# Optimization experiments

Hardware: AMD Instinct MI355X
Metric: run time of the kernel (lower is better)

Reference implementation:

```python
import jax, jax.numpy as jnp
import numpy as np

B, L = 8, 512
D_MODEL, N_HEADS, N_LAYERS = 768, 12, 12
D_HEAD = D_MODEL // N_HEADS
D_FF = 4 * D_MODEL
NUM_LABELS = 1000
PATCH_DIM = 16 * 16 * 3
EPS = 1e-6


def setup_inputs() -> dict:
    key = jax.random.key(0)
    ks = jax.random.split(key, 24)
    d = D_MODEL

    def w(k, shape, fan_in):
        return (jax.random.normal(k, shape, jnp.float32) / np.sqrt(fan_in)).astype(jnp.float32)

    return {
        'patch': jax.random.normal(ks[0], (B, L, PATCH_DIM), jnp.float32),
        'box': jax.random.uniform(ks[1], (B, L, 4), jnp.float32),
        'patch_W': w(ks[2], (PATCH_DIM, d), PATCH_DIM),
        'patch_b': jnp.zeros((d,), jnp.float32),
        'box_W': w(ks[3], (d, d), d),
        'box_b': jnp.zeros((d,), jnp.float32),
        'Wq': w(ks[4], (N_LAYERS, d, d), d),
        'Wk': w(ks[5], (N_LAYERS, d, d), d),
        'Wv': w(ks[6], (N_LAYERS, d, d), d),
        'Wo': w(ks[7], (N_LAYERS, d, d), d),
        'attn_norm_w': jnp.ones((N_LAYERS, d), jnp.float32),
        'gate_W': w(ks[8], (N_LAYERS, d, D_FF), d),
        'hidden_W': w(ks[9], (N_LAYERS, d, D_FF), d),
        'ffn_out_W': w(ks[10], (N_LAYERS, D_FF, d), D_FF),
        'ffn_norm_w': jnp.ones((N_LAYERS, d), jnp.float32),
        'reward_norm_w': jnp.ones((d,), jnp.float32),
        'reward_W': w(ks[11], (d, 2), d),
        'reward_b': jnp.zeros((2,), jnp.float32),
        'label_norm_w': jnp.ones((d,), jnp.float32),
        'label_W': w(ks[12], (d, NUM_LABELS), d),
        'label_b': jnp.zeros((NUM_LABELS,), jnp.float32),
        'box_norm_w': jnp.ones((d,), jnp.float32),
        'boxh_W': w(ks[13], (d, 4), d),
        'boxh_b': jnp.zeros((4,), jnp.float32),
    }


def _rmsnorm(x, wgt):
    return x * jax.lax.rsqrt(jnp.mean(x * x, axis=-1, keepdims=True) + EPS) * wgt


def _rope(x, cos, sin):
    # x: [b, n, l, dh]; consecutive pairs form complex numbers (view_as_complex)
    xr, xi = x[..., 0::2], x[..., 1::2]
    out_r = xr * cos - xi * sin
    out_i = xr * sin + xi * cos
    return jnp.stack((out_r, out_i), axis=-1).reshape(x.shape)


def _forward(patch, box, patch_W, patch_b, box_W, box_b, Wq, Wk, Wv, Wo,
             attn_norm_w, gate_W, hidden_W, ffn_out_W, ffn_norm_w,
             reward_norm_w, reward_W, reward_b, label_norm_w, label_W, label_b,
             box_norm_w, boxh_W, boxh_b):
    b, l, _ = patch.shape
    d = D_MODEL
    # StackedSinusoidalEmbedding(d_model, 4): d_stack = d/4, theta over d_stack/2 freqs
    d_stack = d // 4
    theta_box = 1.0 / (10000.0 ** (2.0 * jnp.arange(d_stack // 2, dtype=jnp.float32) / d_stack))
    ang = box[..., None] * theta_box  # [b, l, 4, d_stack/2]
    box_sin = jnp.stack((jnp.cos(ang), jnp.sin(ang)), axis=-1).reshape(b, l, d)

    x = (patch @ patch_W + patch_b) + (box_sin @ box_W + box_b)

    # RoPE tables and causal mask (constants)
    theta = 1.0 / (10000.0 ** (2.0 * jnp.arange(D_HEAD // 2, dtype=jnp.float32) / D_HEAD))
    pos_ang = jnp.arange(l, dtype=jnp.float32)[:, None] * theta  # [l, dh/2]
    cos, sin = jnp.cos(pos_ang), jnp.sin(pos_ang)
    mask = jnp.triu(jnp.full((l, l), -jnp.inf, dtype=jnp.float32), 1)
    scale = jnp.float32(np.sqrt(D_HEAD))

    def block(h, p):
        wq, wk, wv, wo, anw, gw, hw, ow, fnw = p
        hn = _rmsnorm(h, anw)
        q = (hn @ wq).reshape(b, l, N_HEADS, D_HEAD).transpose(0, 2, 1, 3)
        k = (hn @ wk).reshape(b, l, N_HEADS, D_HEAD).transpose(0, 2, 1, 3)
        v = (hn @ wv).reshape(b, l, N_HEADS, D_HEAD).transpose(0, 2, 1, 3)
        scores = jnp.einsum('bnld,bnmd->bnlm', _rope(q, cos, sin), _rope(k, cos, sin)) / scale
        attn = jax.nn.softmax(scores + mask, axis=-1)
        o = jnp.einsum('bnlm,bnmd->bnld', attn, v).transpose(0, 2, 1, 3).reshape(b, l, d)
        h = h + o @ wo
        hn = _rmsnorm(h, fnw)
        h = h + (jax.nn.silu(hn @ gw) * (hn @ hw)) @ ow
        return h, None

    x, _ = jax.lax.scan(block, x, (Wq, Wk, Wv, Wo, attn_norm_w, gate_W, hidden_W, ffn_out_W, ffn_norm_w))

    reward = _rmsnorm(x, reward_norm_w) @ reward_W + reward_b
    label = _rmsnorm(x, label_norm_w) @ label_W + label_b
    box_out = _rmsnorm(x, box_norm_w) @ boxh_W + boxh_b
    return reward, label, box_out


def reference(patch, box, patch_W, patch_b, box_W, box_b, Wq, Wk, Wv, Wo,
              attn_norm_w, gate_W, hidden_W, ffn_out_W, ffn_norm_w,
              reward_norm_w, reward_W, reward_b, label_norm_w, label_W, label_b,
              box_norm_w, boxh_W, boxh_b):
    return _forward(patch, box, patch_W, patch_b, box_W, box_b, Wq, Wk, Wv, Wo,
                    attn_norm_w, gate_W, hidden_W, ffn_out_W, ffn_norm_w,
                    reward_norm_w, reward_W, reward_b, label_norm_w, label_W, label_b,
                    box_norm_w, boxh_W, boxh_b)
```

## Files before the change

### kernel.cpp

```cpp
#include <hip/hip_runtime.h>
#include <math.h>
#include <type_traits>

#define B_   8
#define L_   512
#define MTOK 4096
#define D_   768
#define NH_  12
#define DH_  64
#define DFF_ 3072
#define NL_  12

typedef unsigned short u16;
typedef __attribute__((ext_vector_type(4))) float f32x4;
typedef __attribute__((ext_vector_type(8))) short i16x8;
typedef __attribute__((ext_vector_type(8))) __bf16 b16x8;

template <typename A, typename = void>
struct PickFrag { using type = i16x8; };
template <typename A>
struct PickFrag<A, std::void_t<decltype(__builtin_amdgcn_mfma_f32_16x16x32_bf16(
    std::declval<A>(), std::declval<A>(), std::declval<f32x4>(), 0, 0, 0))>> {
  using type = A;
};
using frag_t = typename PickFrag<b16x8>::type;

#if __has_builtin(__builtin_amdgcn_global_load_lds)
#define HAS_GLDS 1
#else
#define HAS_GLDS 0
#endif

__device__ inline u16 f2bf(float f) {
    unsigned u = __float_as_uint(f);
    unsigned r = u + 0x7fffu + ((u >> 16) & 1u);
    return (u16)(r >> 16);
}
__device__ inline float bf2f(u16 b) { return __uint_as_float(((unsigned)b) << 16); }

__device__ inline void bar_raw() {
    asm volatile("" ::: "memory");
    __builtin_amdgcn_s_barrier();
    asm volatile("" ::: "memory");
}

__global__ void k_box_sin(u16* __restrict__ emb, const float* __restrict__ box) {
    int idx = blockIdx.x * blockDim.x + threadIdx.x;
    if (idx >= MTOK * D_) return;
    int t = idx / D_, d = idx % D_;
    int c = d / 192, r = d % 192, j = r >> 1;
    float theta = __expf(-(float)j * (9.210340371976184f / 96.0f));
    float ang = box[t * 4 + c] * theta;
    emb[(size_t)t * 1536 + 768 + d] = f2bf((r & 1) ? sinf(ang) : cosf(ang));
}

__global__ void k_cast(u16* __restrict__ emb, const float* __restrict__ in, int n4) {
    int i = blockIdx.x * blockDim.x + threadIdx.x;
    if (i >= n4) return;
    int t = i / 192, c4 = (i % 192) * 4;
    float4 v = *reinterpret_cast<const float4*>(in + (size_t)t * 768 + c4);
    unsigned lo = (unsigned)f2bf(v.x) | ((unsigned)f2bf(v.y) << 16);
    unsigned hi = (unsigned)f2bf(v.z) | ((unsigned)f2bf(v.w) << 16);
    *reinterpret_cast<uint2*>(emb + (size_t)t * 1536 + c4) = make_uint2(lo, hi);
}

__global__ void k_addb(float* __restrict__ dst, const float* __restrict__ a,
                       const float* __restrict__ b) {
    int i = blockIdx.x * blockDim.x + threadIdx.x;
    if (i < D_) dst[i] = a[i] + b[i];
}

__global__ __launch_bounds__(256) void k_convT(u16* __restrict__ dst,
                                               const float* __restrict__ src,
                                               int K, int N, int ld, int rs,
                                               int ro, int co) {
    __shared__ float t[32][33];
    int bn = blockIdx.x * 32;
    int bk = blockIdx.y * 32;
    int tx = threadIdx.x % 32, ty = threadIdx.x / 32;
    #pragma unroll
    for (int i = 0; i < 4; ++i) {
        int k = bk + ty + i * 8;
        int n = bn + tx;
        t[ty + i * 8][tx] = (n < N) ? src[(size_t)k * N + n] : 0.0f;
    }
    __syncthreads();
    #pragma unroll
    for (int i = 0; i < 4; ++i) {
        int n = bn + ty + i * 8;
        int k = bk + tx;
        dst[(size_t)(n * rs + ro) * ld + co + k] = f2bf(t[tx][ty + i * 8]);
    }
}

__global__ __launch_bounds__(256) void k_convT_b1(u16* __restrict__ dst,
                                                  const float* __restrict__ src,
                                                  int K, int N) {
    __shared__ float t[32][33];
    const float* s = src + (size_t)blockIdx.z * K * N;
    u16* d = dst + (size_t)blockIdx.z * K * N;
    int bn = blockIdx.x * 32, bk = blockIdx.y * 32;
    int tx = threadIdx.x % 32, ty = threadIdx.x / 32;
    #pragma unroll
    for (int i = 0; i < 4; ++i)
        t[ty + i * 8][tx] = s[(size_t)(bk + ty + i * 8) * N + bn + tx];
    __syncthreads();
    #pragma unroll
    for (int i = 0; i < 4; ++i) {
        int n = bn + ty + i * 8, k = bk + tx;
        d[(size_t)n * K + k] = f2bf(t[tx][ty + i * 8]);
    }
}

__global__ __launch_bounds__(256) void k_convT_qkv(u16* __restrict__ dst,
                                                   const float* __restrict__ s0,
                                                   const float* __restrict__ s1,
                                                   const float* __restrict__ s2) {
    __shared__ float t[32][33];
    int ly = blockIdx.z / 3, which = blockIdx.z % 3;
    const float* src = (which == 0 ? s0 : (which == 1 ? s1 : s2)) + (size_t)ly * 768 * 768;
    u16* d = dst + ((size_t)ly * 3 + which) * 768 * 768;
    int bn = blockIdx.x * 32, bk = blockIdx.y * 32;
    int tx = threadIdx.x % 32, ty = threadIdx.x / 32;
    #pragma unroll
    for (int i = 0; i < 4; ++i)
        t[ty + i * 8][tx] = src[(size_t)(bk + ty + i * 8) * 768 + bn + tx];
    __syncthreads();
    #pragma unroll
    for (int i = 0; i < 4; ++i) {
        int n = bn + ty + i * 8, k = bk + tx;
        d[(size_t)n * 768 + k] = f2bf(t[tx][ty + i * 8]);
    }
}

__global__ __launch_bounds__(256) void k_convT_gh(u16* __restrict__ dst,
                                                  const float* __restrict__ g,
                                                  const float* __restrict__ h) {
    __shared__ float t[32][33];
    int ly = blockIdx.z >> 1, which = blockIdx.z & 1;
    const float* src = (which ? h : g) + (size_t)ly * 768 * 3072;
    u16* d = dst + (size_t)ly * 6144 * 768;
    int ro = which * 16;
    int bn = blockIdx.x * 32, bk = blockIdx.y * 32;
    int tx = threadIdx.x % 32, ty = threadIdx.x / 32;
    #pragma unroll
    for (int i = 0; i < 4; ++i)
        t[ty + i * 8][tx] = src[(size_t)(bk + ty + i * 8) * 3072 + bn + tx];
    __syncthreads();
    #pragma unroll
    for (int i = 0; i < 4; ++i) {
        int n = bn + ty + i * 8, k = bk + tx;
        int row = ((n >> 4) << 5) + (n & 15) + ro;
        d[(size_t)row * 768 + k] = f2bf(t[tx][ty + i * 8]);
    }
}

__global__ __launch_bounds__(256) void k_rmsnorm(u16* __restrict__ out,
                                                 const float* __restrict__ in,
                                                 const float* __restrict__ w) {
    int t = blockIdx.x;
    const float* x = in + (size_t)t * D_;
    float ss = 0.f;
    for (int i = threadIdx.x; i < D_; i += 256) { float v = x[i]; ss += v * v; }
    for (int off = 32; off > 0; off >>= 1) ss += __shfl_down(ss, off);
    __shared__ float red[4];
    int wid = threadIdx.x >> 6, lane = threadIdx.x & 63;
    if (lane == 0) red[wid] = ss;
    __syncthreads();
    float tot = red[0] + red[1] + red[2] + red[3];
    float inv = rsqrtf(tot / (float)D_ + 1e-6f);
    for (int i = threadIdx.x; i < D_; i += 256)
        out[(size_t)t * D_ + i] = f2bf(x[i] * inv * w[i]);
}

template <int S>
__global__ __launch_bounds__(256) void k_fused_rr(float* __restrict__ h,
                                                  const float* __restrict__ part,
                                                  u16* __restrict__ hn,
                                                  const float* __restrict__ w) {
    int t = blockIdx.x;
    size_t base = (size_t)t * D_;
    float x[3];
    float ss = 0.f;
    #pragma unroll
    for (int c = 0; c < 3; ++c) {
        int i = threadIdx.x + c * 256;
        float v = h[base + i];
        #pragma unroll
        for (int s = 0; s < S; ++s)
            v += part[(size_t)s * MTOK * D_ + base + i];
        x[c] = v;
        h[base + i] = v;
        ss += v * v;
    }
    for (int off = 32; off > 0; off >>= 1) ss += __shfl_down(ss, off);
    __shared__ float red[4];
    int wid = threadIdx.x >> 6, lane = threadIdx.x & 63;
    if (lane == 0) red[wid] = ss;
    __syncthreads();
    float tot = red[0] + red[1] + red[2] + red[3];
    float inv = rsqrtf(tot / (float)D_ + 1e-6f);
    #pragma unroll
    for (int c = 0; c < 3; ++c) {
        int i = threadIdx.x + c * 256;
        hn[base + i] = f2bf(x[c] * inv * w[i]);
    }
}

__global__ void k_rope_tab(float* __restrict__ tab) {
    int idx = blockIdx.x * blockDim.x + threadIdx.x;
    if (idx >= L_ * 32) return;
    int l = idx >> 5, j = idx & 31;
    float theta = __expf(-(float)j * (9.210340371976184f / 32.0f));
    float s, c;
    sincosf((float)l * theta, &s, &c);
    tab[idx * 2] = c;
    tab[idx * 2 + 1] = s;
}

__global__ __launch_bounds__(256) void k_qkvprep(u16* __restrict__ qh,
                                                 u16* __restrict__ kh,
                                                 u16* __restrict__ vT,
                                                 const u16* __restrict__ qkv,
                                                 const float* __restrict__ tab) {
    int bh = blockIdx.x, lb = blockIdx.y;
    int b = bh / NH_, hh = bh % NH_;
    int tid = threadIdx.x;
    int r = tid >> 3, c8 = (tid & 7) * 8;
    int l = lb * 32 + r;
    size_t rowbase = ((size_t)(b * L_ + l)) * 2304 + hh * 64 + c8;

    float2 cs[4];
    #pragma unroll
    for (int p = 0; p < 4; ++p)
        cs[p] = *reinterpret_cast<const float2*>(tab + ((size_t)l * 32 + (c8 >> 1) + p) * 2);

    {
        uint4 v4 = *reinterpret_cast<const uint4*>(qkv + rowbase);
        const u16* pv = reinterpret_cast<const u16*>(&v4);
        u16 out[8];
        #pragma unroll
        for (int p = 0; p < 4; ++p) {
            float xr = bf2f(pv[2 * p]), xi = bf2f(pv[2 * p + 1]);
            out[2 * p]     = f2bf((xr * cs[p].x - xi * cs[p].y) * 0.125f);
            out[2 * p + 1] = f2bf((xr * cs[p].y + xi * cs[p].x) * 0.125f);
        }
        *reinterpret_cast<uint4*>(qh + ((size_t)bh * L_ + l) * 64 + c8) =
            *reinterpret_cast<uint4*>(out);
    }
    {
        uint4 v4 = *reinterpret_cast<const uint4*>(qkv + rowbase + 768);
        const u16* pv = reinterpret_cast<const u16*>(&v4);
        u16 out[8];
        #pragma unroll
        for (int p = 0; p < 4; ++p) {
            float xr = bf2f(pv[2 * p]), xi = bf2f(pv[2 * p + 1]);
            out[2 * p]     = f2bf(xr * cs[p].x - xi * cs[p].y);
            out[2 * p + 1] = f2bf(xr * cs[p].y + xi * cs[p].x);
        }
        *reinterpret_cast<uint4*>(kh + ((size_t)bh * L_ + l) * 64 + c8) =
            *reinterpret_cast<uint4*>(out);
    }
    __shared__ u16 ts[64][40];
    {
        uint4 v4 = *reinterpret_cast<const uint4*>(qkv + rowbase + 1536);
        const u16* pv = reinterpret_cast<const u16*>(&v4);
        #pragma unroll
        for (int j = 0; j < 8; ++j) ts[c8 + j][r] = pv[j];
    }
    __syncthreads();
    {
        int d = tid >> 2, l0 = (tid & 3) * 8;
        uint4 o4 = *reinterpret_cast<const uint4*>(&ts[d][l0]);
        *reinterpret_cast<uint4*>(vT + ((size_t)bh * 64 + d) * L_ + lb * 32 + l0) = o4;
    }
}

template <int MODE>
__global__ __launch_bounds__(256) void k_gemm_bf16(void* __restrict__ Cp,
                                                   const u16* __restrict__ A,
                                                   const u16* __restrict__ BT,
                                                   const float* __restrict__ bias,
                                                   int K, int Nout, int ldC) {
    __shared__ u16 As[2][128 * 32];
    __shared__ u16 Bs[2][128 * 32];
    int tid = threadIdx.x;
    int wid = tid >> 6, lane = tid & 63;

    int nx = gridDim.x, ny = gridDim.y, nz = gridDim.z;
    int bid = ((blockIdx.z * ny) + blockIdx.y) * nx + blockIdx.x;
    int nwg = nx * ny * nz;
    int cpx = nwg >> 3;
    int swz = (bid & 7) * cpx + (bid >> 3);
    int sk  = swz / (nx * ny);
    int rem = swz % (nx * ny);
    int by = rem / nx, bx = rem % nx;
    int row0 = by * 128, col0 = bx * 128;
    int wr = wid >> 1, wc = wid & 1;

    int Klen = K / nz;
    int kbeg = sk * Klen;

    int c0 = wid * 128 + lane;
    int c1 = c0 + 64;
    int r0 = c0 >> 2, kc0 = (c0 & 3) * 8;
    int r1 = c1 >> 2, kc1 = (c1 & 3) * 8;
    const u16* gA0 = A  + (size_t)(row0 + r0) * K + kbeg + kc0;
    const u16* gA1 = A  + (size_t)(row0 + r1) * K + kbeg + kc1;
    const u16* gB0 = BT + (size_t)(col0 + r0) * K + kbeg + kc0;
    const u16* gB1 = BT + (size_t)(col0 + r1) * K + kbeg + kc1;

    auto stage = [&](int buf, int kt) {
#if HAS_GLDS
        __builtin_amdgcn_global_load_lds(
            (const __attribute__((address_space(1))) void*)(gA0 + kt),
            (__attribute__((address_space(3))) void*)&As[buf][c0 * 8], 16, 0, 0);
        __builtin_amdgcn_global_load_lds(
            (const __attribute__((address_space(1))) void*)(gA1 + kt),
            (__attribute__((address_space(3))) void*)&As[buf][c1 * 8], 16, 0, 0);
        __builtin_amdgcn_global_load_lds(
            (const __attribute__((address_space(1))) void*)(gB0 + kt),
            (__attribute__((address_space(3))) void*)&Bs[buf][c0 * 8], 16, 0, 0);
        __builtin_amdgcn_global_load_lds(
            (const __attribute__((address_space(1))) void*)(gB1 + kt),
            (__attribute__((address_space(3))) void*)&Bs[buf][c1 * 8], 16, 0, 0);
#else
        *reinterpret_cast<uint4*>(&As[buf][c0 * 8]) = *reinterpret_cast<const uint4*>(gA0 + kt);
        *reinterpret_cast<uint4*>(&As[buf][c1 * 8]) = *reinterpret_cast<const uint4*>(gA1 + kt);
        *reinterpret_cast<uint4*>(&Bs[buf][c0 * 8]) = *reinterpret_cast<const uint4*>(gB0 + kt);
        *reinterpret_cast<uint4*>(&Bs[buf][c1 * 8]) = *reinterpret_cast<const uint4*>(gB1 + kt);
#endif
    };

    f32x4 acc[4][4] = {};
    int lrow = lane & 15, lk = (lane >> 4) * 8;

    stage(0, 0);
    int cur = 0;
    for (int kt = 0; kt < Klen; kt += 32) {
        bool has_next = (kt + 32 < Klen);
        if (has_next) stage(cur ^ 1, kt + 32);
        if (has_next) asm volatile("s_waitcnt vmcnt(4) lgkmcnt(0)" ::: "memory");
        else          asm volatile("s_waitcnt vmcnt(0) lgkmcnt(0)" ::: "memory");
        __builtin_amdgcn_sched_barrier(0);
        bar_raw();
        frag_t af[4], bfr[4];
        #pragma unroll
        for (int m = 0; m < 4; ++m)
            af[m] = *reinterpret_cast<const frag_t*>(&As[cur][(wr * 64 + m * 16 + lrow) * 32 + lk]);
        #pragma unroll
        for (int n = 0; n < 4; ++n)
            bfr[n] = *reinterpret_cast<const frag_t*>(&Bs[cur][(wc * 64 + n * 16 + lrow) * 32 + lk]);
        #pragma unroll
        for (int m = 0; m < 4; ++m)
            #pragma unroll
            for (int n = 0; n < 4; ++n)
                acc[m][n] = __builtin_amdgcn_mfma_f32_16x16x32_bf16(af[m], bfr[n], acc[m][n], 0, 0, 0);
        bar_raw();
        cur ^= 1;
    }

    int lcol = lane & 15, rb = (lane >> 4) * 4;
    if (MODE == 5) {
        #pragma unroll
        for (int m = 0; m < 4; ++m) {
            #pragma unroll
            for (int np = 0; np < 2; ++np) {
                int ocol = (col0 >> 1) + wc * 32 + np * 16 + lcol;
                #pragma unroll
                for (int e = 0; e < 4; ++e) {
                    int row = row0 + wr * 64 + m * 16 + rb + e;
                    float g = acc[m][2 * np][e], hv = acc[m][2 * np + 1][e];
                    float s = g / (1.0f + __expf(-g));
                    ((u16*)Cp)[(size_t)row * ldC + ocol] = f2bf(s * hv);
                }
            }
        }
        return;
    }

    float* Cpart = (MODE == 4)
        ? ((float*)Cp + (size_t)sk * (size_t)(ny * 128) * ldC) : (float*)Cp;
    #pragma unroll
    for (int m = 0; m < 4; ++m) {
        #pragma unroll
        for (int n = 0; n < 4; ++n) {
            int col = col0 + wc * 64 + n * 16 + lcol;
            if (col >= Nout) continue;
            #pragma unroll
            for (int e = 0; e < 4; ++e) {
                int row = row0 + wr * 64 + m * 16 + rb + e;
                float v = acc[m][n][e];
                size_t off = (size_t)row * ldC + col;
                if (MODE == 0) {
                    if (bias) v += bias[col];
                    ((float*)Cp)[off] = v;
                } else if (MODE == 3) {
                    ((u16*)Cp)[off] = f2bf(v);
                } else if (MODE == 4) {
                    Cpart[off] = v;
                }
            }
        }
    }
}

__global__ __launch_bounds__(256) void k_attn3(u16* __restrict__ o,
                                               const u16* __restrict__ qh,
                                               const u16* __restrict__ kh,
                                               const u16* __restrict__ vT) {
    int bh = blockIdx.x, qb = blockIdx.y;
    int b = bh / NH_, hh = bh % NH_;
    int tid = threadIdx.x, wid = tid >> 6, lane = tid & 63;
    __shared__ u16 Qs[64][72], Ks[64][72], Vs[64][72], Ps[64][72];

    #pragma unroll
    for (int i = 0; i < 2; ++i) {
        int idx = tid + i * 256;
        int r = idx >> 3, c8 = (idx & 7) * 8;
        uint4 v4 = *reinterpret_cast<const uint4*>(
            qh + ((size_t)bh * L_ + qb * 64 + r) * 64 + c8);
        *reinterpret_cast<uint4*>(&Qs[r][c8]) = v4;
    }
    __syncthreads();

    int lr = lane & 15, lg = lane >> 4;
    frag_t aq[2];
    #pragma unroll
    for (int kd = 0; kd < 2; ++kd)
        aq[kd] = *reinterpret_cast<const frag_t*>(&Qs[wid * 16 + lr][kd * 32 + lg * 8]);

    f32x4 accO[4] = {};
    float M[4], S[4];
    #pragma unroll
    for (int e = 0; e < 4; ++e) { M[e] = -INFINITY; S[e] = 0.f; }

    for (int kb = 0; kb <= qb; ++kb) {
        __syncthreads();
        #pragma unroll
        for (int i = 0; i < 2; ++i) {
            int idx = tid + i * 256;
            int r = idx >> 3, c8 = (idx & 7) * 8;
            *reinterpret_cast<uint4*>(&Ks[r][c8]) = *reinterpret_cast<const uint4*>(
                kh + ((size_t)bh * L_ + kb * 64 + r) * 64 + c8);
            *reinterpret_cast<uint4*>(&Vs[r][c8]) = *reinterpret_cast<const uint4*>(
                vT + ((size_t)bh * 64 + r) * L_ + kb * 64 + c8);
        }
        __syncthreads();

        f32x4 sv[4];
        #pragma unroll
        for (int ct = 0; ct < 4; ++ct) {
            frag_t bk0 = *reinterpret_cast<const frag_t*>(&Ks[ct * 16 + lr][lg * 8]);
            frag_t bk1 = *reinterpret_cast<const frag_t*>(&Ks[ct * 16 + lr][32 + lg * 8]);
            f32x4 z = {0.f, 0.f, 0.f, 0.f};
            z = __builtin_amdgcn_mfma_f32_16x16x32_bf16(aq[0], bk0, z, 0, 0, 0);
            sv[ct] = __builtin_amdgcn_mfma_f32_16x16x32_bf16(aq[1], bk1, z, 0, 0, 0);
        }

        bool diag = (kb == qb);
        float esc[4];
        #pragma unroll
        for (int e = 0; e < 4; ++e) {
            int qg = qb * 64 + wid * 16 + lg * 4 + e;
            float mx = -1e30f;
            #pragma unroll
            for (int ct = 0; ct < 4; ++ct) {
                float s = sv[ct][e];
                if (diag && (kb * 64 + ct * 16 + lr > qg)) s = -1e30f;
                sv[ct][e] = s;
                mx = fmaxf(mx, s);
            }
            #pragma unroll
            for (int msk = 8; msk; msk >>= 1) mx = fmaxf(mx, __shfl_xor(mx, msk));
            float newM = fmaxf(M[e], mx);
            float ps = 0.f;
            #pragma unroll
            for (int ct = 0; ct < 4; ++ct) {
                float p = __expf(sv[ct][e] - newM);
                sv[ct][e] = p;
                ps += p;
            }
            #pragma unroll
            for (int msk = 8; msk; msk >>= 1) ps += __shfl_xor(ps, msk);
            esc[e] = __expf(M[e] - newM);
            S[e] = S[e] * esc[e] + ps;
            M[e] = newM;
        }
        #pragma unroll
        for (int dt = 0; dt < 4; ++dt)
            #pragma unroll
            for (int e = 0; e < 4; ++e) accO[dt][e] *= esc[e];

        #pragma unroll
        for (int ct = 0; ct < 4; ++ct)
            #pragma unroll
            for (int e = 0; e < 4; ++e)
                Ps[wid * 16 + lg * 4 + e][ct * 16 + lr] = f2bf(sv[ct][e]);

        frag_t pa0 = *reinterpret_cast<const frag_t*>(&Ps[wid * 16 + lr][lg * 8]);
        frag_t pa1 = *reinterpret_cast<const frag_t*>(&Ps[wid * 16 + lr][32 + lg * 8]);
        #pragma unroll
        for (int dt = 0; dt < 4; ++dt) {
            frag_t bv0 = *reinterpret_cast<const frag_t*>(&Vs[dt * 16 + lr][lg * 8]);
            frag_t bv1 = *reinterpret_cast<const frag_t*>(&Vs[dt * 16 + lr][32 + lg * 8]);
            accO[dt] = __builtin_amdgcn_mfma_f32_16x16x32_bf16(pa0, bv0, accO[dt], 0, 0, 0);
            accO[dt] = __builtin_amdgcn_mfma_f32_16x16x32_bf16(pa1, bv1, accO[dt], 0, 0, 0);
        }
    }

    #pragma unroll
    for (int dt = 0; dt < 4; ++dt) {
        #pragma unroll
        for (int e = 0; e < 4; ++e) {
            int row = b * L_ + qb * 64 + wid * 16 + lg * 4 + e;
            o[(size_t)row * D_ + hh * 64 + dt * 16 + lr] = f2bf(accO[dt][e] / S[e]);
        }
    }
}

__global__ __launch_bounds__(256) void k_heads3(float* __restrict__ out_reward,
                                                float* __restrict__ out_box,
                                                const float* __restrict__ h,
                                                const float* __restrict__ rnw,
                                                const float* __restrict__ rW,
                                                const float* __restrict__ rb,
                                                const float* __restrict__ bnw,
                                                const float* __restrict__ bW,
                                                const float* __restrict__ bb) {
    int t = blockIdx.x;
    size_t base = (size_t)t * D_;
    float x[3];
    float ss = 0.f;
    #pragma unroll
    for (int c = 0; c < 3; ++c) {
        int i = threadIdx.x + c * 256;
        x[c] = h[base + i];
        ss += x[c] * x[c];
    }
    for (int off = 32; off > 0; off >>= 1) ss += __shfl_down(ss, off);
    __shared__ float red[4];
    int wid = threadIdx.x >> 6, lane = threadIdx.x & 63;
    if (lane == 0) red[wid] = ss;
    __syncthreads();
    float inv = rsqrtf((red[0] + red[1] + red[2] + red[3]) / (float)D_ + 1e-6f);

    float a[6] = {};
    #pragma unroll
    for (int c = 0; c < 3; ++c) {
        int i = threadIdx.x + c * 256;
        float xr = x[c] * inv;
        float xw = xr * rnw[i];
        a[0] += xw * rW[i * 2];
        a[1] += xw * rW[i * 2 + 1];
        float xb = xr * bnw[i];
        #pragma unroll
        for (int j = 0; j < 4; ++j) a[2 + j] += xb * bW[i * 4 + j];
    }
    #pragma unroll
    for (int j = 0; j < 6; ++j)
        for (int off = 32; off > 0; off >>= 1) a[j] += __shfl_down(a[j], off);
    __shared__ float red2[4][6];
    if (lane == 0)
        #pragma unroll
        for (int j = 0; j < 6; ++j) red2[wid][j] = a[j];
    __syncthreads();
    if (threadIdx.x < 6) {
        float s = red2[0][threadIdx.x] + red2[1][threadIdx.x] +
                  red2[2][threadIdx.x] + red2[3][threadIdx.x];
        if (threadIdx.x < 2) out_reward[(size_t)t * 2 + threadIdx.x] = s + rb[threadIdx.x];
        else                 out_box[(size_t)t * 4 + threadIdx.x - 2] = s + bb[threadIdx.x - 2];
    }
}

extern "C" void kernel_launch(void* const* d_in, const int* in_sizes, int n_in,
                              void* d_out, int out_size, void* d_ws, size_t ws_size,
                              hipStream_t stream) {
    const float* patch        = (const float*)d_in[0];
    const float* box          = (const float*)d_in[1];
    const float* patch_W      = (const float*)d_in[2];
    const float* patch_b      = (const float*)d_in[3];
    const float* box_W        = (const float*)d_in[4];
    const float* box_b        = (const float*)d_in[5];
    const float* Wq           = (const float*)d_in[6];
    const float* Wk           = (const float*)d_in[7];
    const float* Wv           = (const float*)d_in[8];
    const float* Wo           = (const float*)d_in[9];
    const float* attn_norm_w  = (const float*)d_in[10];
    const float* gate_W       = (const float*)d_in[11];
    const float* hidden_W     = (const float*)d_in[12];
    const float* ffn_out_W    = (const float*)d_in[13];
    const float* ffn_norm_w   = (const float*)d_in[14];
    const float* reward_norm_w= (const float*)d_in[15];
    const float* reward_W     = (const float*)d_in[16];
    const float* reward_b     = (const float*)d_in[17];
    const float* label_norm_w = (const float*)d_in[18];
    const float* label_W      = (const float*)d_in[19];
    const float* label_b      = (const float*)d_in[20];
    const float* box_norm_w   = (const float*)d_in[21];
    const float* boxh_W       = (const float*)d_in[22];
    const float* boxh_b       = (const float*)d_in[23];

    char* w = (char*)d_ws;
    auto alloc = [&](size_t bytes) { char* p = w; w += (bytes + 255) & ~(size_t)255; return p; };

    u16*  wqkv_a = (u16*)alloc((size_t)NL_ * 2304 * 768 * 2);
    u16*  wo_a   = (u16*)alloc((size_t)NL_ * 768 * 768 * 2);
    u16*  wgh_a  = (u16*)alloc((size_t)NL_ * 6144 * 768 * 2);
    u16*  wfo_a  = (u16*)alloc((size_t)NL_ * 768 * 3072 * 2);
    u16*  wcat   = (u16*)alloc((size_t)768 * 1536 * 2);
    u16*  wlab   = (u16*)alloc((size_t)1024 * 768 * 2);
    float* bias_c= (float*)alloc((size_t)768 * 4);
    u16*  emb    = (u16*)alloc((size_t)MTOK * 1536 * 2);
    float* h     = (float*)alloc((size_t)MTOK * D_ * 4);
    u16*  hn_bf  = (u16*)alloc((size_t)MTOK * D_ * 2);
    u16*  qkv_bf = (u16*)alloc((size_t)MTOK * 2304 * 2);
    u16*  vT     = (u16*)alloc((size_t)MTOK * D_ * 2);
    float* tab   = (float*)alloc((size_t)L_ * 32 * 2 * 4);
    u16*  o_bf   = (u16*)alloc((size_t)MTOK * D_ * 2);
    u16*  ga_bf  = (u16*)alloc((size_t)MTOK * DFF_ * 2);
    float* part  = (float*)alloc((size_t)4 * MTOK * D_ * 4);

    u16* qh = emb;
    u16* kh = emb + (size_t)MTOK * 768;

    dim3 blk(256);

    k_convT<<<dim3(24, 24), blk, 0, stream>>>(wcat, patch_W, 768, 768, 1536, 1, 0, 0);
    k_convT<<<dim3(24, 24), blk, 0, stream>>>(wcat, box_W,   768, 768, 1536, 1, 0, 768);
    k_convT<<<dim3(32, 24), blk, 0, stream>>>(wlab, label_W, 768, 1000, 768, 1, 0, 0);
    k_addb<<<3, blk, 0, stream>>>(bias_c, patch_b, box_b);
    k_rope_tab<<<(L_ * 32 + 255) / 256, blk, 0, stream>>>(tab);
    k_convT_qkv<<<dim3(24, 24, 36), blk, 0, stream>>>(wqkv_a, Wq, Wk, Wv);
    k_convT_b1<<<dim3(24, 24, 12), blk, 0, stream>>>(wo_a, Wo, 768, 768);
    k_convT_gh<<<dim3(96, 24, 24), blk, 0, stream>>>(wgh_a, gate_W, hidden_W);
    k_convT_b1<<<dim3(24, 96, 12), blk, 0, stream>>>(wfo_a, ffn_out_W, 3072, 768);
    k_cast<<<(MTOK * 768 / 4 + 255) / 256, blk, 0, stream>>>(emb, patch, MTOK * 768 / 4);
    k_box_sin<<<(MTOK * D_ + 255) / 256, blk, 0, stream>>>(emb, box);

    k_gemm_bf16<0><<<dim3(6, 32), blk, 0, stream>>>(h, emb, wcat, bias_c, 1536, 768, 768);
    k_rmsnorm<<<MTOK, blk, 0, stream>>>(hn_bf, h, attn_norm_w);

    for (int ly = 0; ly < NL_; ++ly) {
        const u16* wqkv = wqkv_a + (size_t)ly * 2304 * 768;
        const u16* wo_l = wo_a   + (size_t)ly * 768 * 768;
        const u16* wgh  = wgh_a  + (size_t)ly * 6144 * 768;
        const u16* wfo  = wfo_a  + (size_t)ly * 768 * 3072;
        const float* fnw = ffn_norm_w + (size_t)ly * D_;
        const float* nxt = (ly + 1 < NL_) ? attn_norm_w + (size_t)(ly + 1) * D_
                                          : label_norm_w;

        k_gemm_bf16<3><<<dim3(18, 32), blk, 0, stream>>>(qkv_bf, hn_bf, wqkv, nullptr, 768, 2304, 2304);
        k_qkvprep<<<dim3(96, 16), blk, 0, stream>>>(qh, kh, vT, qkv_bf, tab);
        k_attn3<<<dim3(96, 8), blk, 0, stream>>>(o_bf, qh, kh, vT);
        k_gemm_bf16<4><<<dim3(6, 32, 2), blk, 0, stream>>>(part, o_bf, wo_l, nullptr, 768, 768, 768);
        k_fused_rr<2><<<MTOK, blk, 0, stream>>>(h, part, hn_bf, fnw);

        k_gemm_bf16<5><<<dim3(48, 32), blk, 0, stream>>>(ga_bf, hn_bf, wgh, nullptr, 768, 6144, 3072);
        k_gemm_bf16<4><<<dim3(6, 32, 4), blk, 0, stream>>>(part, ga_bf, wfo, nullptr, 3072, 768, 768);
        k_fused_rr<4><<<MTOK, blk, 0, stream>>>(h, part, hn_bf, nxt);
    }

    float* out_reward = (float*)d_out;
    float* out_label  = out_reward + (size_t)MTOK * 2;
    float* out_box    = out_label + (size_t)MTOK * 1000;

    k_gemm_bf16<0><<<dim3(8, 32), blk, 0, stream>>>(out_label, hn_bf, wlab, label_b, 768, 1000, 1000);
    k_heads3<<<MTOK, blk, 0, stream>>>(out_reward, out_box, h,
                                       reward_norm_w, reward_W, reward_b,
                                       box_norm_w, boxh_W, boxh_b);
}
```

Measured before the change: 2.466 ms.

## Fuse RoPE, Q scaling and V transpose into QKV GEMM epilogue

Removes the separate qkvprep kernel per layer. The QKV GEMM epilogue now applies RoPE and the Q scale, writing head-major Q/K directly, and transposes V through shared memory into vT. It also widens the weight-transpose kernels to 64-element K tiles with 16-byte stores and adds s_setprio around the attention MFMA blocks. The trade-off is scattered 2-byte stores and per-element table loads in the Q/K epilogue, plus extra syncs for the V path.

```diff
diff --git a/kernel.cpp b/kernel.cpp
--- a/kernel.cpp
+++ b/kernel.cpp
@@ -93,66 +93,76 @@
     }
 }
 
-__global__ __launch_bounds__(256) void k_convT_b1(u16* __restrict__ dst,
-                                                  const float* __restrict__ src,
-                                                  int K, int N) {
-    __shared__ float t[32][33];
+
+__global__ __launch_bounds__(256) void k_convT64(u16* __restrict__ dst,
+                                                 const float* __restrict__ src,
+                                                 int K, int N) {
+    __shared__ float ts[32][65];
     const float* s = src + (size_t)blockIdx.z * K * N;
     u16* d = dst + (size_t)blockIdx.z * K * N;
-    int bn = blockIdx.x * 32, bk = blockIdx.y * 32;
-    int tx = threadIdx.x % 32, ty = threadIdx.x / 32;
-    #pragma unroll
-    for (int i = 0; i < 4; ++i)
-        t[ty + i * 8][tx] = s[(size_t)(bk + ty + i * 8) * N + bn + tx];
-    __syncthreads();
-    #pragma unroll
-    for (int i = 0; i < 4; ++i) {
-        int n = bn + ty + i * 8, k = bk + tx;
-        d[(size_t)n * K + k] = f2bf(t[tx][ty + i * 8]);
-    }
-}
-
-__global__ __launch_bounds__(256) void k_convT_qkv(u16* __restrict__ dst,
-                                                   const float* __restrict__ s0,
-                                                   const float* __restrict__ s1,
-                                                   const float* __restrict__ s2) {
-    __shared__ float t[32][33];
+    int bn = blockIdx.x * 32, bk = blockIdx.y * 64;
+    int t = threadIdx.x, rn = t & 31;
+    #pragma unroll
+    for (int p = 0; p < 8; ++p) {
+        int k = p * 8 + (t >> 5);
+        ts[rn][k] = s[(size_t)(bk + k) * N + bn + rn];
+    }
+    __syncthreads();
+    int n = t >> 3, kc = (t & 7) * 8;
+    u16 tmp[8];
+    #pragma unroll
+    for (int j = 0; j < 8; ++j) tmp[j] = f2bf(ts[n][kc + j]);
+    *reinterpret_cast<uint4*>(&d[(size_t)(bn + n) * K + bk + kc]) =
+        *reinterpret_cast<uint4*>(tmp);
+}
+
+__global__ __launch_bounds__(256) void k_convT64_qkv(u16* __restrict__ dst,
+                                                     const float* __restrict__ s0,
+                                                     const float* __restrict__ s1,
+                                                     const float* __restrict__ s2) {
+    __shared__ float ts[32][65];
     int ly = blockIdx.z / 3, which = blockIdx.z % 3;
-    const float* src = (which == 0 ? s0 : (which == 1 ? s1 : s2)) + (size_t)ly * 768 * 768;
+    const float* s = (which == 0 ? s0 : (which == 1 ? s1 : s2)) + (size_t)ly * 768 * 768;
     u16* d = dst + ((size_t)ly * 3 + which) * 768 * 768;
-    int bn = blockIdx.x * 32, bk = blockIdx.y * 32;
-    int tx = threadIdx.x % 32, ty = threadIdx.x / 32;
-    #pragma unroll
-    for (int i = 0; i < 4; ++i)
-        t[ty + i * 8][tx] = src[(size_t)(bk + ty + i * 8) * 768 + bn + tx];
-    __syncthreads();
-    #pragma unroll
-    for (int i = 0; i < 4; ++i) {
-        int n = bn + ty + i * 8, k = bk + tx;
-        d[(size_t)n * 768 + k] = f2bf(t[tx][ty + i * 8]);
-    }
-}
-
-__global__ __launch_bounds__(256) void k_convT_gh(u16* __restrict__ dst,
-                                                  const float* __restrict__ g,
-                                                  const float* __restrict__ h) {
-    __shared__ float t[32][33];
+    int bn = blockIdx.x * 32, bk = blockIdx.y * 64;
+    int t = threadIdx.x, rn = t & 31;
+    #pragma unroll
+    for (int p = 0; p < 8; ++p) {
+        int k = p * 8 + (t >> 5);
+        ts[rn][k] = s[(size_t)(bk + k) * 768 + bn + rn];
+    }
+    __syncthreads();
+    int n = t >> 3, kc = (t & 7) * 8;
+    u16 tmp[8];
+    #pragma unroll
+    for (int j = 0; j < 8; ++j) tmp[j] = f2bf(ts[n][kc + j]);
+    *reinterpret_cast<uint4*>(&d[(size_t)(bn + n) * 768 + bk + kc]) =
+        *reinterpret_cast<uint4*>(tmp);
+}
+
+__global__ __launch_bounds__(256) void k_convT64_gh(u16* __restrict__ dst,
+                                                    const float* __restrict__ g,
+                                                    const float* __restrict__ h) {
+    __shared__ float ts[32][65];
     int ly = blockIdx.z >> 1, which = blockIdx.z & 1;
-    const float* src = (which ? h : g) + (size_t)ly * 768 * 3072;
+    const float* s = (which ? h : g) + (size_t)ly * 768 * 3072;
     u16* d = dst + (size_t)ly * 6144 * 768;
-    int ro = which * 16;
-    int bn = blockIdx.x * 32, bk = blockIdx.y * 32;
-    int tx = threadIdx.x % 32, ty = threadIdx.x / 32;
-    #pragma unroll
-    for (int i = 0; i < 4; ++i)
-        t[ty + i * 8][tx] = src[(size_t)(bk + ty + i * 8) * 3072 + bn + tx];
-    __syncthreads();
-    #pragma unroll
-    for (int i = 0; i < 4; ++i) {
-        int n = bn + ty + i * 8, k = bk + tx;
-        int row = ((n >> 4) << 5) + (n & 15) + ro;
-        d[(size_t)row * 768 + k] = f2bf(t[tx][ty + i * 8]);
-    }
+    int bn = blockIdx.x * 32, bk = blockIdx.y * 64;
+    int t = threadIdx.x, rn = t & 31;
+    #pragma unroll
+    for (int p = 0; p < 8; ++p) {
+        int k = p * 8 + (t >> 5);
+        ts[rn][k] = s[(size_t)(bk + k) * 3072 + bn + rn];
+    }
+    __syncthreads();
+    int n = t >> 3, kc = (t & 7) * 8;
+    int ng = bn + n;
+    int row = ((ng >> 4) << 5) + (ng & 15) + which * 16;
+    u16 tmp[8];
+    #pragma unroll
+    for (int j = 0; j < 8; ++j) tmp[j] = f2bf(ts[n][kc + j]);
+    *reinterpret_cast<uint4*>(&d[(size_t)row * 768 + bk + kc]) =
+        *reinterpret_cast<uint4*>(tmp);
 }
 
 __global__ __launch_bounds__(256) void k_rmsnorm(u16* __restrict__ out,
@@ -218,72 +228,13 @@
     tab[idx * 2 + 1] = s;
 }
 
-__global__ __launch_bounds__(256) void k_qkvprep(u16* __restrict__ qh,
-                                                 u16* __restrict__ kh,
-                                                 u16* __restrict__ vT,
-                                                 const u16* __restrict__ qkv,
-                                                 const float* __restrict__ tab) {
-    int bh = blockIdx.x, lb = blockIdx.y;
-    int b = bh / NH_, hh = bh % NH_;
-    int tid = threadIdx.x;
-    int r = tid >> 3, c8 = (tid & 7) * 8;
-    int l = lb * 32 + r;
-    size_t rowbase = ((size_t)(b * L_ + l)) * 2304 + hh * 64 + c8;
-
-    float2 cs[4];
-    #pragma unroll
-    for (int p = 0; p < 4; ++p)
-        cs[p] = *reinterpret_cast<const float2*>(tab + ((size_t)l * 32 + (c8 >> 1) + p) * 2);
-
-    {
-        uint4 v4 = *reinterpret_cast<const uint4*>(qkv + rowbase);
-        const u16* pv = reinterpret_cast<const u16*>(&v4);
-        u16 out[8];
-        #pragma unroll
-        for (int p = 0; p < 4; ++p) {
-            float xr = bf2f(pv[2 * p]), xi = bf2f(pv[2 * p + 1]);
-            out[2 * p]     = f2bf((xr * cs[p].x - xi * cs[p].y) * 0.125f);
-            out[2 * p + 1] = f2bf((xr * cs[p].y + xi * cs[p].x) * 0.125f);
-        }
-        *reinterpret_cast<uint4*>(qh + ((size_t)bh * L_ + l) * 64 + c8) =
-            *reinterpret_cast<uint4*>(out);
-    }
-    {
-        uint4 v4 = *reinterpret_cast<const uint4*>(qkv + rowbase + 768);
-        const u16* pv = reinterpret_cast<const u16*>(&v4);
-        u16 out[8];
-        #pragma unroll
-        for (int p = 0; p < 4; ++p) {
-            float xr = bf2f(pv[2 * p]), xi = bf2f(pv[2 * p + 1]);
-            out[2 * p]     = f2bf(xr * cs[p].x - xi * cs[p].y);
-            out[2 * p + 1] = f2bf(xr * cs[p].y + xi * cs[p].x);
-        }
-        *reinterpret_cast<uint4*>(kh + ((size_t)bh * L_ + l) * 64 + c8) =
-            *reinterpret_cast<uint4*>(out);
-    }
-    __shared__ u16 ts[64][40];
-    {
-        uint4 v4 = *reinterpret_cast<const uint4*>(qkv + rowbase + 1536);
-        const u16* pv = reinterpret_cast<const u16*>(&v4);
-        #pragma unroll
-        for (int j = 0; j < 8; ++j) ts[c8 + j][r] = pv[j];
-    }
-    __syncthreads();
-    {
-        int d = tid >> 2, l0 = (tid & 3) * 8;
-        uint4 o4 = *reinterpret_cast<const uint4*>(&ts[d][l0]);
-        *reinterpret_cast<uint4*>(vT + ((size_t)bh * 64 + d) * L_ + lb * 32 + l0) = o4;
-    }
-}
-
 template <int MODE>
 __global__ __launch_bounds__(256) void k_gemm_bf16(void* __restrict__ Cp,
                                                    const u16* __restrict__ A,
                                                    const u16* __restrict__ BT,
                                                    const float* __restrict__ bias,
                                                    int K, int Nout, int ldC) {
-    __shared__ u16 As[2][128 * 32];
-    __shared__ u16 Bs[2][128 * 32];
+    __shared__ u16 smem[16384];
     int tid = threadIdx.x;
     int wid = tid >> 6, lane = tid & 63;
 
@@ -311,24 +262,26 @@
     const u16* gB1 = BT + (size_t)(col0 + r1) * K + kbeg + kc1;
 
     auto stage = [&](int buf, int kt) {
+        u16* Asb = smem + buf * 4096;
+        u16* Bsb = smem + 8192 + buf * 4096;
 #if HAS_GLDS
         __builtin_amdgcn_global_load_lds(
             (const __attribute__((address_space(1))) void*)(gA0 + kt),
-            (__attribute__((address_space(3))) void*)&As[buf][c0 * 8], 16, 0, 0);
+            (__attribute__((address_space(3))) void*)&Asb[c0 * 8], 16, 0, 0);
         __builtin_amdgcn_global_load_lds(
             (const __attribute__((address_space(1))) void*)(gA1 + kt),
-            (__attribute__((address_space(3))) void*)&As[buf][c1 * 8], 16, 0, 0);
+            (__attribute__((address_space(3))) void*)&Asb[c1 * 8], 16, 0, 0);
         __builtin_amdgcn_global_load_lds(
             (const __attribute__((address_space(1))) void*)(gB0 + kt),
-            (__attribute__((address_space(3))) void*)&Bs[buf][c0 * 8], 16, 0, 0);
+            (__attribute__((address_space(3))) void*)&Bsb[c0 * 8], 16, 0, 0);
         __builtin_amdgcn_global_load_lds(
             (const __attribute__((address_space(1))) void*)(gB1 + kt),
-            (__attribute__((address_space(3))) void*)&Bs[buf][c1 * 8], 16, 0, 0);
+            (__attribute__((address_space(3))) void*)&Bsb[c1 * 8], 16, 0, 0);
 #else
-        *reinterpret_cast<uint4*>(&As[buf][c0 * 8]) = *reinterpret_cast<const uint4*>(gA0 + kt);
-        *reinterpret_cast<uint4*>(&As[buf][c1 * 8]) = *reinterpret_cast<const uint4*>(gA1 + kt);
-        *reinterpret_cast<uint4*>(&Bs[buf][c0 * 8]) = *reinterpret_cast<const uint4*>(gB0 + kt);
-        *reinterpret_cast<uint4*>(&Bs[buf][c1 * 8]) = *reinterpret_cast<const uint4*>(gB1 + kt);
+        *reinterpret_cast<uint4*>(&Asb[c0 * 8]) = *reinterpret_cast<const uint4*>(gA0 + kt);
+        *reinterpret_cast<uint4*>(&Asb[c1 * 8]) = *reinterpret_cast<const uint4*>(gA1 + kt);
+        *reinterpret_cast<uint4*>(&Bsb[c0 * 8]) = *reinterpret_cast<const uint4*>(gB0 + kt);
+        *reinterpret_cast<uint4*>(&Bsb[c1 * 8]) = *reinterpret_cast<const uint4*>(gB1 + kt);
 #endif
     };
 
@@ -344,13 +297,15 @@
         else          asm volatile("s_waitcnt vmcnt(0) lgkmcnt(0)" ::: "memory");
         __builtin_amdgcn_sched_barrier(0);
         bar_raw();
+        const u16* Asb = smem + cur * 4096;
+        const u16* Bsb = smem + 8192 + cur * 4096;
         frag_t af[4], bfr[4];
         #pragma unroll
         for (int m = 0; m < 4; ++m)
-            af[m] = *reinterpret_cast<const frag_t*>(&As[cur][(wr * 64 + m * 16 + lrow) * 32 + lk]);
+            af[m] = *reinterpret_cast<const frag_t*>(&Asb[(wr * 64 + m * 16 + lrow) * 32 + lk]);
         #pragma unroll
         for (int n = 0; n < 4; ++n)
-            bfr[n] = *reinterpret_cast<const frag_t*>(&Bs[cur][(wc * 64 + n * 16 + lrow) * 32 + lk]);
+            bfr[n] = *reinterpret_cast<const frag_t*>(&Bsb[(wc * 64 + n * 16 + lrow) * 32 + lk]);
         #pragma unroll
         for (int m = 0; m < 4; ++m)
             #pragma unroll
@@ -361,6 +316,74 @@
     }
 
     int lcol = lane & 15, rb = (lane >> 4) * 4;
+
+    if (MODE == 6) {
+        u16* qkvh = (u16*)Cp;
+        const float* tab = bias;
+        if (col0 >= 1536) {
+            int head_base = (col0 - 1536) >> 6;
+            int bb = row0 >> 9;
+            int l0 = row0 & 511;
+            #pragma unroll
+            for (int pass = 0; pass < 2; ++pass) {
+                if (wc == pass) {
+                    #pragma unroll
+                    for (int m = 0; m < 4; ++m) {
+                        #pragma unroll
+                        for (int n = 0; n < 4; ++n) {
+                            int dl = n * 16 + lcol;
+                            int rl = wr * 64 + m * 16 + rb;
+                            u16 tmp[4];
+                            #pragma unroll
+                            for (int e = 0; e < 4; ++e) tmp[e] = f2bf(acc[m][n][e]);
+                            *reinterpret_cast<uint2*>(&smem[dl * 136 + rl]) =
+                                *reinterpret_cast<uint2*>(tmp);
+                        }
+                    }
+                }
+                __syncthreads();
+                int head = head_base + pass;
+                size_t vbase = (size_t)2 * MTOK * 768 +
+                               ((size_t)(bb * NH_ + head) * 64) * 512;
+                #pragma unroll
+                for (int it = 0; it < 4; ++it) {
+                    int dd = it * 16 + (tid >> 4);
+                    int rr = (tid & 15) * 8;
+                    uint4 v4 = *reinterpret_cast<const uint4*>(&smem[dd * 136 + rr]);
+                    *reinterpret_cast<uint4*>(&qkvh[vbase + (size_t)dd * 512 + l0 + rr]) = v4;
+                }
+                __syncthreads();
+            }
+        } else {
+            int sec = col0 / 768;
+            float qscale = (sec == 0) ? 0.125f : 1.0f;
+            #pragma unroll
+            for (int m = 0; m < 4; ++m) {
+                #pragma unroll
+                for (int n = 0; n < 4; ++n) {
+                    int col = col0 + wc * 64 + n * 16 + lcol;
+                    int head = (col % 768) >> 6;
+                    int d = col & 63;
+                    #pragma unroll
+                    for (int e = 0; e < 4; ++e) {
+                        int row = row0 + wr * 64 + m * 16 + rb + e;
+                        int bb = row >> 9, l = row & 511;
+                        float v = acc[m][n][e];
+                        float p = __shfl_xor(v, 1);
+                        float2 cs = *reinterpret_cast<const float2*>(
+                            tab + ((size_t)l * 32 + (d >> 1)) * 2);
+                        float r = (d & 1) ? (p * cs.y + v * cs.x)
+                                          : (v * cs.x - p * cs.y);
+                        r *= qscale;
+                        qkvh[(size_t)sec * MTOK * 768 +
+                             ((size_t)(bb * NH_ + head) * 512 + l) * 64 + d] = f2bf(r);
+                    }
+                }
+            }
+        }
+        return;
+    }
+
     if (MODE == 5) {
         #pragma unroll
         for (int m = 0; m < 4; ++m) {
@@ -449,6 +472,7 @@
         __syncthreads();
 
         f32x4 sv[4];
+        __builtin_amdgcn_s_setprio(1);
         #pragma unroll
         for (int ct = 0; ct < 4; ++ct) {
             frag_t bk0 = *reinterpret_cast<const frag_t*>(&Ks[ct * 16 + lr][lg * 8]);
@@ -457,6 +481,7 @@
             z = __builtin_amdgcn_mfma_f32_16x16x32_bf16(aq[0], bk0, z, 0, 0, 0);
             sv[ct] = __builtin_amdgcn_mfma_f32_16x16x32_bf16(aq[1], bk1, z, 0, 0, 0);
         }
+        __builtin_amdgcn_s_setprio(0);
 
         bool diag = (kb == qb);
         float esc[4];
@@ -500,6 +525,7 @@
 
         frag_t pa0 = *reinterpret_cast<const frag_t*>(&Ps[wid * 16 + lr][lg * 8]);
         frag_t pa1 = *reinterpret_cast<const frag_t*>(&Ps[wid * 16 + lr][32 + lg * 8]);
+        __builtin_amdgcn_s_setprio(1);
         #pragma unroll
         for (int dt = 0; dt < 4; ++dt) {
             frag_t bv0 = *reinterpret_cast<const frag_t*>(&Vs[dt * 16 + lr][lg * 8]);
@@ -507,6 +533,7 @@
             accO[dt] = __builtin_amdgcn_mfma_f32_16x16x32_bf16(pa0, bv0, accO[dt], 0, 0, 0);
             accO[dt] = __builtin_amdgcn_mfma_f32_16x16x32_bf16(pa1, bv1, accO[dt], 0, 0, 0);
         }
+        __builtin_amdgcn_s_setprio(0);
     }
 
     #pragma unroll
@@ -614,15 +641,15 @@
     u16*  emb    = (u16*)alloc((size_t)MTOK * 1536 * 2);
     float* h     = (float*)alloc((size_t)MTOK * D_ * 4);
     u16*  hn_bf  = (u16*)alloc((size_t)MTOK * D_ * 2);
-    u16*  qkv_bf = (u16*)alloc((size_t)MTOK * 2304 * 2);
-    u16*  vT     = (u16*)alloc((size_t)MTOK * D_ * 2);
+    u16*  qkvh   = (u16*)alloc((size_t)MTOK * 2304 * 2);
     float* tab   = (float*)alloc((size_t)L_ * 32 * 2 * 4);
     u16*  o_bf   = (u16*)alloc((size_t)MTOK * D_ * 2);
     u16*  ga_bf  = (u16*)alloc((size_t)MTOK * DFF_ * 2);
     float* part  = (float*)alloc((size_t)4 * MTOK * D_ * 4);
 
-    u16* qh = emb;
-    u16* kh = emb + (size_t)MTOK * 768;
+    u16* qh = qkvh;
+    u16* kh = qkvh + (size_t)MTOK * 768;
+    u16* vT = qkvh + (size_t)2 * MTOK * 768;
 
     dim3 blk(256);
 
@@ -631,10 +658,10 @@
     k_convT<<<dim3(32, 24), blk, 0, stream>>>(wlab, label_W, 768, 1000, 768, 1, 0, 0);
     k_addb<<<3, blk, 0, stream>>>(bias_c, patch_b, box_b);
     k_rope_tab<<<(L_ * 32 + 255) / 256, blk, 0, stream>>>(tab);
-    k_convT_qkv<<<dim3(24, 24, 36), blk, 0, stream>>>(wqkv_a, Wq, Wk, Wv);
-    k_convT_b1<<<dim3(24, 24, 12), blk, 0, stream>>>(wo_a, Wo, 768, 768);
-    k_convT_gh<<<dim3(96, 24, 24), blk, 0, stream>>>(wgh_a, gate_W, hidden_W);
-    k_convT_b1<<<dim3(24, 96, 12), blk, 0, stream>>>(wfo_a, ffn_out_W, 3072, 768);
+    k_convT64_qkv<<<dim3(24, 12, 36), blk, 0, stream>>>(wqkv_a, Wq, Wk, Wv);
+    k_convT64<<<dim3(24, 12, 12), blk, 0, stream>>>(wo_a, Wo, 768, 768);
+    k_convT64_gh<<<dim3(96, 12, 24), blk, 0, stream>>>(wgh_a, gate_W, hidden_W);
+    k_convT64<<<dim3(24, 48, 12), blk, 0, stream>>>(wfo_a, ffn_out_W, 3072, 768);
     k_cast<<<(MTOK * 768 / 4 + 255) / 256, blk, 0, stream>>>(emb, patch, MTOK * 768 / 4);
     k_box_sin<<<(MTOK * D_ + 255) / 256, blk, 0, stream>>>(emb, box);
 
@@ -650,8 +677,7 @@
         const float* nxt = (ly + 1 < NL_) ? attn_norm_w + (size_t)(ly + 1) * D_
                                           : label_norm_w;
 
-        k_gemm_bf16<3><<<dim3(18, 32), blk, 0, stream>>>(qkv_bf, hn_bf, wqkv, nullptr, 768, 2304, 2304);
-        k_qkvprep<<<dim3(96, 16), blk, 0, stream>>>(qh, kh, vT, qkv_bf, tab);
+        k_gemm_bf16<6><<<dim3(18, 32), blk, 0, stream>>>(qkvh, hn_bf, wqkv, tab, 768, 2304, 2304);
         k_attn3<<<dim3(96, 8), blk, 0, stream>>>(o_bf, qh, kh, vT);
         k_gemm_bf16<4><<<dim3(6, 32, 2), blk, 0, stream>>>(part, o_bf, wo_l, nullptr, 768, 768, 768);
         k_fused_rr<2><<<MTOK, blk, 0, stream>>>(h, part, hn_bf, fnw);
```

Measured after the change: 2.317 ms. 1.06x faster.
